# Kernel tuning notes

Measured on AMD Instinct MI355X. Metric: run time of the kernel, lower is better.

The kernel has to match this reference:

```python
import jax, jax.numpy as jnp
import numpy as np

N = 100000   # nodes
E = 1600000  # edges
G = 64       # graphs in batch
C = 8        # num_classes
H = 128      # hidden dim


def _lin(k, out_f, in_f):
    return jax.random.normal(k, (out_f, in_f), jnp.float32) * (1.0 / np.sqrt(in_f))


def setup_inputs() -> dict:
    key = jax.random.key(0)
    ks = jax.random.split(key, 16)
    x = jax.random.normal(ks[0], (N, 5), jnp.float32)
    edge_index = jax.random.randint(ks[1], (2, E), 0, N)
    batch = jnp.sort(jax.random.randint(ks[2], (N,), 0, G))
    exinfo = jax.random.normal(ks[3], (G, 10), jnp.float32)
    return {
        "x": x, "edge_index": edge_index, "batch": batch, "exinfo": exinfo,
        # GraphConv1: 3 -> 128 (PyG GraphConv: lin_root(x) + lin_rel(scatter_add(x_j)))
        "Wroot1": _lin(ks[4], H, 3), "Wrel1": _lin(ks[5], H, 3), "brel1": jnp.zeros((H,), jnp.float32),
        # GraphConv2: 128 -> 128
        "Wroot2": _lin(ks[6], H, H), "Wrel2": _lin(ks[7], H, H), "brel2": jnp.zeros((H,), jnp.float32),
        # MLP head
        "W1": _lin(ks[8], 64, 2 * H + 10), "b1": jnp.zeros((64,), jnp.float32),
        "W2": _lin(ks[9], 32, 64), "b2": jnp.zeros((32,), jnp.float32),
        "W3": _lin(ks[10], C, 32), "b3": jnp.zeros((C,), jnp.float32),
    }


def _graph_conv(x, src, dst, Wroot, Wrel, brel):
    # PyG GraphConv (aggr='add'): out_i = Wrel @ sum_{j->i} x_j + brel + Wroot @ x_i
    agg = jax.ops.segment_sum(x[src], dst, num_segments=x.shape[0])  # [N, F]
    return agg @ Wrel.T + brel + x @ Wroot.T


def reference(x, edge_index, batch, exinfo,
              Wroot1, Wrel1, brel1, Wroot2, Wrel2, brel2,
              W1, b1, W2, b2, W3, b3):
    xs = x[:, 2:5]                              # data.x[:, 2:5]
    src, dst = edge_index[0], edge_index[1]
    x1 = jax.nn.relu(_graph_conv(xs, src, dst, Wroot1, Wrel1, brel1))   # [N, 128]
    x2 = jax.nn.relu(_graph_conv(x1, src, dst, Wroot2, Wrel2, brel2))   # [N, 128]
    h = jnp.concatenate([x1, x2], axis=-1)      # [N, 256]
    g = jax.ops.segment_max(h, batch, num_segments=G)  # global max pool [G, 256]
    g = jnp.concatenate([g, exinfo], axis=-1)   # [G, 266]
    g = jax.nn.relu(g @ W1.T + b1)
    g = jax.nn.relu(g @ W2.T + b2)
    return jax.nn.log_softmax(g @ W3.T + b3, axis=-1)
```

## Files before the change

### kernel.cpp

```cpp
#include <hip/hip_runtime.h>

#define N_NODES 100000
#define N_EDGES 1600000
#define NG 64
#define NC 8
#define HD 128

#define BUCKET_SHIFT 8
#define NB ((N_NODES + 255) >> 8)
#define NCHUNK 256
#define EPC (N_EDGES / NCHUNK)

typedef __attribute__((ext_vector_type(8))) __bf16 bf16x8;
typedef __attribute__((ext_vector_type(4))) float f32x4;
typedef __attribute__((ext_vector_type(2))) float f32x2;


__global__ void bin_hist_k(const int* __restrict__ dst, int* __restrict__ hist) {
  __shared__ int lh[NB];
  int c = blockIdx.x, t = threadIdx.x;
  for (int b = t; b < NB; b += 256) lh[b] = 0;
  __syncthreads();
  int e0 = c * EPC;
  for (int i = t; i < EPC; i += 256) atomicAdd(&lh[dst[e0 + i] >> BUCKET_SHIFT], 1);
  __syncthreads();
  for (int b = t; b < NB; b += 256) hist[c * NB + b] = lh[b];
}

__launch_bounds__(512)
__global__ void base_k(const int* __restrict__ hist, int* __restrict__ bucket_base,
                       int* __restrict__ row_ptr) {
  __shared__ int tot[512];
  int t = threadIdx.x;
  int s = 0;
  if (t < NB)
    for (int c = 0; c < NCHUNK; c++) s += hist[c * NB + t];
  tot[t] = s;
  __syncthreads();
  for (int off = 1; off < 512; off <<= 1) {
    int v = (t >= off) ? tot[t - off] : 0;
    __syncthreads();
    tot[t] += v;
    __syncthreads();
  }
  if (t < NB) bucket_base[t] = tot[t] - s;
  if (t == 0) { bucket_base[NB] = N_EDGES; row_ptr[N_NODES] = N_EDGES; }
}

__global__ void chunk_scan_k(int* __restrict__ hist, const int* __restrict__ bucket_base) {
  int b = blockIdx.x, lane = threadIdx.x;
  int carry = bucket_base[b];
#pragma unroll
  for (int it = 0; it < NCHUNK / 64; it++) {
    int c = it * 64 + lane;
    int v = hist[c * NB + b];
    int s = v;
#pragma unroll
    for (int off = 1; off < 64; off <<= 1) {
      int u = __shfl_up(s, off);
      if (lane >= off) s += u;
    }
    hist[c * NB + b] = carry + s - v;
    carry += __shfl(s, 63);
  }
}

__global__ void scatter_k(const int* __restrict__ src, const int* __restrict__ dst,
                          const int* __restrict__ hist, unsigned int* __restrict__ pairs) {
  __shared__ int loff[NB];
  int c = blockIdx.x, t = threadIdx.x;
  for (int b = t; b < NB; b += 256) loff[b] = hist[c * NB + b];
  __syncthreads();
  int e0 = c * EPC;
  for (int i = t; i < EPC; i += 256) {
    int d = dst[e0 + i], s = src[e0 + i];
    int pos = atomicAdd(&loff[d >> BUCKET_SHIFT], 1);
    pairs[pos] = ((unsigned int)s << 8) | (unsigned int)(d & 255);
  }
}

__global__ void bucket_csr_k(const unsigned int* __restrict__ pairs,
                             const int* __restrict__ bucket_base,
                             int* __restrict__ row_ptr, int* __restrict__ csr) {
  __shared__ int cnt[256];
  __shared__ int start[256];
  __shared__ int wsum[4];
  int b = blockIdx.x, t = threadIdx.x, lane = t & 63, wid = t >> 6;
  int nb0 = b << BUCKET_SHIFT;
  int beg = bucket_base[b], end = bucket_base[b + 1];
  cnt[t] = 0;
  __syncthreads();
  for (int i = beg + t; i < end; i += 256) atomicAdd(&cnt[pairs[i] & 255u], 1);
  __syncthreads();
  int v = cnt[t];
  int s = v;
#pragma unroll
  for (int off = 1; off < 64; off <<= 1) {
    int u = __shfl_up(s, off);
    if (lane >= off) s += u;
  }
  if (lane == 63) wsum[wid] = s;
  __syncthreads();
  if (t == 0) {
    int a = 0;
    for (int j = 0; j < 4; j++) { int x = wsum[j]; wsum[j] = a; a += x; }
  }
  __syncthreads();
  int excl = wsum[wid] + s - v;
  start[t] = excl;
  if (nb0 + t < N_NODES) row_ptr[nb0 + t] = beg + excl;
  cnt[t] = 0;
  __syncthreads();
  for (int i = beg + t; i < end; i += 256) {
    unsigned int p = pairs[i];
    int li = p & 255u;
    int pos = beg + start[li] + atomicAdd(&cnt[li], 1);
    csr[pos] = (int)(p >> 8);
  }
}


__global__ void pack_xs_k(const float* __restrict__ x, float4* __restrict__ xs4) {
  int i = blockIdx.x * 256 + threadIdx.x;
  if (i < N_NODES) {
    const float* xp = x + (size_t)i * 5;
    xs4[i] = make_float4(xp[2], xp[3], xp[4], 0.f);
  }
}


__global__ void conv1_k(const float4* __restrict__ xs4, const int* __restrict__ row_ptr,
                        const int* __restrict__ csr, const float* __restrict__ Wroot1,
                        const float* __restrict__ Wrel1, const float* __restrict__ brel1,
                        __bf16* __restrict__ xcat) {
  int node = blockIdx.x * 4 + (threadIdx.x >> 6);
  if (node >= N_NODES) return;
  int lane = threadIdx.x & 63;
  int beg = row_ptr[node], end = row_ptr[node + 1];
  float a0 = 0.f, a1 = 0.f, a2 = 0.f;
  for (int e = beg + lane; e < end; e += 64) {
    float4 v = xs4[csr[e]];
    a0 += v.x; a1 += v.y; a2 += v.z;
  }
#pragma unroll
  for (int m = 1; m < 64; m <<= 1) {
    a0 += __shfl_xor(a0, m);
    a1 += __shfl_xor(a1, m);
    a2 += __shfl_xor(a2, m);
  }
  float4 rv = xs4[node];
  __bf16* orow = xcat + (size_t)node * 256 + 128;
#pragma unroll
  for (int hh = 0; hh < 2; hh++) {
    int h = lane + hh * 64;
    float v = brel1[h]
            + a0 * Wrel1[h * 3 + 0] + a1 * Wrel1[h * 3 + 1] + a2 * Wrel1[h * 3 + 2]
            + rv.x * Wroot1[h * 3 + 0] + rv.y * Wroot1[h * 3 + 1] + rv.z * Wroot1[h * 3 + 2];
    orow[h] = (__bf16)fmaxf(v, 0.f);
  }
}


#define LDROW(s) (*((const uint4*)(xcat + (size_t)(s) * 256 + 128) + f))
#define ACC8(u) \
  acc2[0] += (f32x2){__uint_as_float((u).x << 16), __uint_as_float((u).x & 0xffff0000u)}; \
  acc2[1] += (f32x2){__uint_as_float((u).y << 16), __uint_as_float((u).y & 0xffff0000u)}; \
  acc2[2] += (f32x2){__uint_as_float((u).z << 16), __uint_as_float((u).z & 0xffff0000u)}; \
  acc2[3] += (f32x2){__uint_as_float((u).w << 16), __uint_as_float((u).w & 0xffff0000u)};

__global__ void agg2_k(const int* __restrict__ row_ptr, const int* __restrict__ csr,
                       __bf16* xcat) {
  int node = blockIdx.x * 4 + (threadIdx.x >> 6);
  if (node >= N_NODES) return;
  int lane = threadIdx.x & 63;
  int g = lane >> 4, f = lane & 15;
  int beg = row_ptr[node], end = row_ptr[node + 1];
  int deg = end - beg;
  int idx = (lane < deg) ? csr[beg + lane] : 0;
  f32x2 acc2[4];
#pragma unroll
  for (int k = 0; k < 4; k++) acc2[k] = (f32x2){0.f, 0.f};
  int dmain = deg < 64 ? deg : 64;
  int j = 0;
  for (; j + 16 <= dmain; j += 16) {
    int s0 = __shfl(idx, j + g);
    int s1 = __shfl(idx, j + 4 + g);
    int s2 = __shfl(idx, j + 8 + g);
    int s3 = __shfl(idx, j + 12 + g);
    uint4 u0 = LDROW(s0);
    uint4 u1 = LDROW(s1);
    uint4 u2 = LDROW(s2);
    uint4 u3 = LDROW(s3);
    ACC8(u0) ACC8(u1) ACC8(u2) ACC8(u3)
  }
  if (j + 8 <= dmain) {
    int s0 = __shfl(idx, j + g);
    int s1 = __shfl(idx, j + 4 + g);
    uint4 u0 = LDROW(s0);
    uint4 u1 = LDROW(s1);
    ACC8(u0) ACC8(u1)
    j += 8;
  }
  if (j + 4 <= dmain) {
    int s0 = __shfl(idx, j + g);
    uint4 u0 = LDROW(s0);
    ACC8(u0)
    j += 4;
  }
  {
    int rem = dmain - j;
    int s0 = __shfl(idx, j + (g < rem ? g : 0));
    if (g < rem) {
      uint4 u0 = LDROW(s0);
      ACC8(u0)
    }
  }
  for (int e = beg + 64; e < end; e += 4) {
    int m = end - e;
    int s0 = csr[e + (g < m ? g : 0)];
    if (g < m) {
      uint4 u0 = LDROW(s0);
      ACC8(u0)
    }
  }
#pragma unroll
  for (int k = 0; k < 4; k++) {
    acc2[k].x += __shfl_xor(acc2[k].x, 16);
    acc2[k].y += __shfl_xor(acc2[k].y, 16);
    acc2[k].x += __shfl_xor(acc2[k].x, 32);
    acc2[k].y += __shfl_xor(acc2[k].y, 32);
  }
  if (g == 0) {
    uint4 o;
    o.x = (__float_as_uint((float)(__bf16)acc2[0].x) >> 16) | (__float_as_uint((float)(__bf16)acc2[0].y) & 0xffff0000u);
    o.y = (__float_as_uint((float)(__bf16)acc2[1].x) >> 16) | (__float_as_uint((float)(__bf16)acc2[1].y) & 0xffff0000u);
    o.z = (__float_as_uint((float)(__bf16)acc2[2].x) >> 16) | (__float_as_uint((float)(__bf16)acc2[2].y) & 0xffff0000u);
    o.w = (__float_as_uint((float)(__bf16)acc2[3].x) >> 16) | (__float_as_uint((float)(__bf16)acc2[3].y) & 0xffff0000u);
    *((uint4*)(xcat + (size_t)node * 256) + f) = o;
  }
}


__global__ void build_wc_k(const float* __restrict__ Wrel2, const float* __restrict__ Wroot2,
                           __bf16* __restrict__ Wc) {
  int i = blockIdx.x * 256 + threadIdx.x;
  int h = i >> 8, k = i & 255;
  float v = (k < 128) ? Wrel2[h * 128 + k] : Wroot2[h * 128 + (k - 128)];
  Wc[i] = (__bf16)v;
}


__launch_bounds__(512, 4)
__global__ void gemm2_k(const __bf16* __restrict__ xcat, const __bf16* __restrict__ Wc,
                        const float* __restrict__ brel2, const int* __restrict__ batch,
                        unsigned int* __restrict__ gout) {
  __shared__ char Blds[128 * 256 * 2];
  int t = threadIdx.x;
  for (int i = t; i < 4096; i += 512) {
    uint4 v = ((const uint4*)Wc)[i];
    int byte = i * 16;
    int sw = byte ^ (((byte >> 9) & 7) << 4);
    *(uint4*)(Blds + sw) = v;
  }
  __syncthreads();
  int wid = t >> 6, lane = t & 63;
  int nb = (blockIdx.x * 8 + wid) * 32;
  if (nb >= N_NODES) return;
  int r = lane & 15, ko = lane >> 4;
  const __bf16* arow0 = xcat + (size_t)(nb + r) * 256 + ko * 8;
  const __bf16* arow1 = arow0 + 16 * 256;
  f32x4 acc0[8], acc1[8];
#pragma unroll
  for (int i = 0; i < 8; i++) {
    acc0[i] = (f32x4){0.f, 0.f, 0.f, 0.f};
    acc1[i] = (f32x4){0.f, 0.f, 0.f, 0.f};
  }
#pragma unroll
  for (int kb = 0; kb < 256; kb += 32) {
    bf16x8 a0 = *(const bf16x8*)(arow0 + kb);
    bf16x8 a1 = *(const bf16x8*)(arow1 + kb);
#pragma unroll
    for (int ht = 0; ht < 8; ht++) {
      int h = ht * 16 + r;
      int byte = h * 512 + ko * 16 + kb * 2;
      bf16x8 b = *(const bf16x8*)(Blds + (byte ^ ((r & 7) << 4)));
      acc0[ht] = __builtin_amdgcn_mfma_f32_16x16x32_bf16(a0, b, acc0[ht], 0, 0, 0);
      acc1[ht] = __builtin_amdgcn_mfma_f32_16x16x32_bf16(a1, b, acc1[ht], 0, 0, 0);
    }
  }
  int gfirst = batch[nb], glast = batch[nb + 31];
  if (gfirst == glast) {
    unsigned int* gp = gout + gfirst * 256 + 128;
#pragma unroll
    for (int ht = 0; ht < 8; ht++) {
      float bias = brel2[ht * 16 + r];
      float m = 0.f;
#pragma unroll
      for (int rr = 0; rr < 4; rr++) {
        m = fmaxf(m, acc0[ht][rr] + bias);
        m = fmaxf(m, acc1[ht][rr] + bias);
      }
      m = fmaxf(m, __shfl_xor(m, 16));
      m = fmaxf(m, __shfl_xor(m, 32));
      if (ko == 0) atomicMax(&gp[ht * 16 + r], __float_as_uint(m));
    }
  } else {
    int g0[4], g1[4];
#pragma unroll
    for (int rr = 0; rr < 4; rr++) {
      g0[rr] = batch[nb + ko * 4 + rr];
      g1[rr] = batch[nb + 16 + ko * 4 + rr];
    }
#pragma unroll
    for (int ht = 0; ht < 8; ht++) {
      int h = ht * 16 + r;
      float bias = brel2[h];
#pragma unroll
      for (int rr = 0; rr < 4; rr++) {
        atomicMax(&gout[g0[rr] * 256 + 128 + h],
                  __float_as_uint(fmaxf(acc0[ht][rr] + bias, 0.f)));
        atomicMax(&gout[g1[rr] * 256 + 128 + h],
                  __float_as_uint(fmaxf(acc1[ht][rr] + bias, 0.f)));
      }
    }
  }
}


__global__ void segmax1_k(const __bf16* __restrict__ xcat, const int* __restrict__ batch,
                          unsigned int* __restrict__ g) {
  int t = threadIdx.x;
  int f = t & 63;
  int s = t >> 6;
  int n0 = blockIdx.x * 256;
  float m0 = 0.f, m1 = 0.f;
  int cur = -1;
  int n1 = n0 + 256 < N_NODES ? n0 + 256 : N_NODES;
  for (int n = n0 + s; n < n1; n += 4) {
    int b = batch[n];
    if (b != cur) {
      if (cur >= 0) {
        atomicMax(&g[cur * 256 + 2 * f], __float_as_uint(m0));
        atomicMax(&g[cur * 256 + 2 * f + 1], __float_as_uint(m1));
      }
      cur = b; m0 = 0.f; m1 = 0.f;
    }
    unsigned int u = ((const unsigned int*)(xcat + (size_t)n * 256 + 128))[f];
    m0 = fmaxf(m0, __uint_as_float(u << 16));
    m1 = fmaxf(m1, __uint_as_float(u & 0xffff0000u));
  }
  if (cur >= 0) {
    atomicMax(&g[cur * 256 + 2 * f], __float_as_uint(m0));
    atomicMax(&g[cur * 256 + 2 * f + 1], __float_as_uint(m1));
  }
}


__global__ void head1_k(const float* __restrict__ g, const float* __restrict__ exinfo,
                        const float* __restrict__ W1, const float* __restrict__ b1,
                        float* __restrict__ g1) {
  int gg = blockIdx.x;
  int t = threadIdx.x;
  int c = t >> 2, q = t & 3;
  const float* w = W1 + c * 266;
  const float* gr = g + gg * 256;
  float s = 0.f;
  for (int k = q * 64; k < q * 64 + 64; k++) s += gr[k] * w[k];
  if (q == 0) {
    const float* er = exinfo + gg * 10;
    for (int k = 0; k < 10; k++) s += er[k] * w[256 + k];
    s += b1[c];
  }
  s += __shfl_xor(s, 1);
  s += __shfl_xor(s, 2);
  if (q == 0) g1[gg * 64 + c] = fmaxf(s, 0.f);
}

__global__ void head2_k(const float* __restrict__ g1, const float* __restrict__ W2,
                        const float* __restrict__ b2, const float* __restrict__ W3,
                        const float* __restrict__ b3, float* __restrict__ out) {
  __shared__ float s1[64 * 64];
  __shared__ float s2[64 * 32];
  int t = threadIdx.x;
  for (int i = t; i < 4096; i += 256) s1[i] = g1[i];
  __syncthreads();
  for (int o = t; o < 2048; o += 256) {
    int r = o >> 5, c = o & 31;
    float s = b2[c];
    for (int k = 0; k < 64; k++) s += s1[r * 64 + k] * W2[c * 64 + k];
    s2[r * 32 + c] = fmaxf(s, 0.f);
  }
  __syncthreads();
  if (t < 64) {
    float lg[8];
#pragma unroll
    for (int c = 0; c < 8; c++) {
      float s = b3[c];
      for (int k = 0; k < 32; k++) s += s2[t * 32 + k] * W3[c * 32 + k];
      lg[c] = s;
    }
    float mx = lg[0];
#pragma unroll
    for (int c = 1; c < 8; c++) mx = fmaxf(mx, lg[c]);
    float se = 0.f;
#pragma unroll
    for (int c = 0; c < 8; c++) se += expf(lg[c] - mx);
    float lse = mx + logf(se);
#pragma unroll
    for (int c = 0; c < 8; c++) out[t * 8 + c] = lg[c] - lse;
  }
}


extern "C" void kernel_launch(void* const* d_in, const int* in_sizes, int n_in,
                              void* d_out, int out_size, void* d_ws, size_t ws_size,
                              hipStream_t stream) {
  const float* x      = (const float*)d_in[0];
  const int*   edge   = (const int*)d_in[1];
  const int*   batch  = (const int*)d_in[2];
  const float* exinfo = (const float*)d_in[3];
  const float* Wroot1 = (const float*)d_in[4];
  const float* Wrel1  = (const float*)d_in[5];
  const float* brel1  = (const float*)d_in[6];
  const float* Wroot2 = (const float*)d_in[7];
  const float* Wrel2  = (const float*)d_in[8];
  const float* brel2  = (const float*)d_in[9];
  const float* W1     = (const float*)d_in[10];
  const float* b1     = (const float*)d_in[11];
  const float* W2     = (const float*)d_in[12];
  const float* b2     = (const float*)d_in[13];
  const float* W3     = (const float*)d_in[14];
  const float* b3     = (const float*)d_in[15];
  const int* src = edge;
  const int* dst = edge + N_EDGES;

  char* p = (char*)d_ws;
  auto alloc = [&](size_t bytes) {
    char* q = p;
    p += (bytes + 511) & ~(size_t)511;
    return (void*)q;
  };
  __bf16*       Wc          = (__bf16*)alloc(128 * 256 * 2);
  unsigned int* g           = (unsigned int*)alloc(64 * 256 * 4);
  float*        g1          = (float*)alloc(64 * 64 * 4);
  float4*       xs4         = (float4*)alloc((size_t)N_NODES * 16);
  int*          hist        = (int*)alloc((size_t)NCHUNK * NB * 4);
  int*          bucket_base = (int*)alloc((size_t)(NB + 1) * 4);
  int*          row_ptr     = (int*)alloc((size_t)(N_NODES + 1) * 4);
  int*          csr         = (int*)alloc((size_t)N_EDGES * 4);
  __bf16*       xcat        = (__bf16*)alloc((size_t)N_NODES * 256 * 2);
  unsigned int* pairs       = (unsigned int*)alloc((size_t)N_EDGES * 4);

  hipMemsetAsync(g, 0, 64 * 256 * 4, stream);
  build_wc_k<<<128, 256, 0, stream>>>(Wrel2, Wroot2, Wc);
  pack_xs_k<<<NB, 256, 0, stream>>>(x, xs4);
  bin_hist_k<<<NCHUNK, 256, 0, stream>>>(dst, hist);
  base_k<<<1, 512, 0, stream>>>(hist, bucket_base, row_ptr);
  chunk_scan_k<<<NB, 64, 0, stream>>>(hist, bucket_base);
  scatter_k<<<NCHUNK, 256, 0, stream>>>(src, dst, hist, pairs);
  bucket_csr_k<<<NB, 256, 0, stream>>>(pairs, bucket_base, row_ptr, csr);
  conv1_k<<<25000, 256, 0, stream>>>(xs4, row_ptr, csr, Wroot1, Wrel1, brel1, xcat);
  agg2_k<<<25000, 256, 0, stream>>>(row_ptr, csr, xcat);
  gemm2_k<<<391, 512, 0, stream>>>(xcat, Wc, brel2, batch, g);
  segmax1_k<<<NB, 256, 0, stream>>>(xcat, batch, g);
  head1_k<<<64, 256, 0, stream>>>((const float*)g, exinfo, W1, b1, g1);
  head2_k<<<1, 256, 0, stream>>>(g1, W2, b2, W3, b3, (float*)d_out);
}
```

Baseline: 215.4 us.

## Gather layer-1 features in FP8 for aggregation, fuse init kernels, parallelize bucket sum

conv1 now also writes an FP8 (e4m3) copy of x1, and the second-layer neighbour aggregation gathers these 128-byte rows instead of 256-byte bf16 rows. This halves the bytes moved by the random gather, but adds quantisation error to the aggregated features. The memset, weight packing and xs packing are merged into one init kernel. The serial per-bucket histogram sum in the single-block scan is replaced by a parallel reduction kernel feeding a smaller scan.

```diff
diff --git a/kernel.cpp b/kernel.cpp
--- a/kernel.cpp
+++ b/kernel.cpp
@@ -15,6 +15,44 @@
 typedef __attribute__((ext_vector_type(4))) float f32x4;
 typedef __attribute__((ext_vector_type(2))) float f32x2;
 
+#if defined(__has_builtin)
+#if __has_builtin(__builtin_amdgcn_cvt_pk_f32_fp8)
+#define HAVE_FP8_CVT 1
+#endif
+#endif
+
+__device__ inline unsigned int f32_to_e4m3(float v) {
+  unsigned int b = __float_as_uint(v);
+  b += 0x00080000u;
+  unsigned int e = b >> 23;
+  if (e < 121) return 0u;
+  unsigned int q = (e > 135) ? 0x7Eu : (((e - 120) << 3) | ((b >> 20) & 7u));
+  return q > 0x7Eu ? 0x7Eu : q;
+}
+
+__device__ inline float e4m3f(unsigned int t) {
+  unsigned int e = (t >> 3) & 0xFu;
+  unsigned int r = ((t & 0x80u) << 24) | ((e + 120u) << 23) | ((t & 7u) << 20);
+  return e ? __uint_as_float(r) : 0.f;
+}
+
+
+__global__ void init_k(const float* __restrict__ x, const float* __restrict__ Wrel2,
+                       const float* __restrict__ Wroot2, float4* __restrict__ xs4,
+                       __bf16* __restrict__ Wc, unsigned int* __restrict__ g) {
+  int i = blockIdx.x * 256 + threadIdx.x;
+  if (i < 64 * 256) g[i] = 0u;
+  if (i < 32768) {
+    int h = i >> 8, k = i & 255;
+    float v = (k < 128) ? Wrel2[h * 128 + k] : Wroot2[h * 128 + (k - 128)];
+    Wc[i] = (__bf16)v;
+  }
+  if (i < N_NODES) {
+    const float* xp = x + (size_t)i * 5;
+    xs4[i] = make_float4(xp[2], xp[3], xp[4], 0.f);
+  }
+}
+
 
 __global__ void bin_hist_k(const int* __restrict__ dst, int* __restrict__ hist) {
   __shared__ int lh[NB];
@@ -27,23 +65,33 @@
   for (int b = t; b < NB; b += 256) hist[c * NB + b] = lh[b];
 }
 
+
+__global__ void bucket_sum_k(const int* __restrict__ hist, int* __restrict__ tot) {
+  __shared__ int ws[4];
+  int b = blockIdx.x, t = threadIdx.x, lane = t & 63, wid = t >> 6;
+  int v = hist[t * NB + b];
+#pragma unroll
+  for (int off = 1; off < 64; off <<= 1) v += __shfl_xor(v, off);
+  if (lane == 0) ws[wid] = v;
+  __syncthreads();
+  if (t == 0) tot[b] = ws[0] + ws[1] + ws[2] + ws[3];
+}
+
 __launch_bounds__(512)
-__global__ void base_k(const int* __restrict__ hist, int* __restrict__ bucket_base,
-                       int* __restrict__ row_ptr) {
-  __shared__ int tot[512];
+__global__ void scan391_k(const int* __restrict__ tot, int* __restrict__ bucket_base,
+                          int* __restrict__ row_ptr) {
+  __shared__ int sm[512];
   int t = threadIdx.x;
-  int s = 0;
-  if (t < NB)
-    for (int c = 0; c < NCHUNK; c++) s += hist[c * NB + t];
-  tot[t] = s;
+  int s = (t < NB) ? tot[t] : 0;
+  sm[t] = s;
   __syncthreads();
   for (int off = 1; off < 512; off <<= 1) {
-    int v = (t >= off) ? tot[t - off] : 0;
+    int v = (t >= off) ? sm[t - off] : 0;
     __syncthreads();
-    tot[t] += v;
+    sm[t] += v;
     __syncthreads();
   }
-  if (t < NB) bucket_base[t] = tot[t] - s;
+  if (t < NB) bucket_base[t] = sm[t] - s;
   if (t == 0) { bucket_base[NB] = N_EDGES; row_ptr[N_NODES] = N_EDGES; }
 }
 
@@ -120,19 +168,10 @@
 }
 
 
-__global__ void pack_xs_k(const float* __restrict__ x, float4* __restrict__ xs4) {
-  int i = blockIdx.x * 256 + threadIdx.x;
-  if (i < N_NODES) {
-    const float* xp = x + (size_t)i * 5;
-    xs4[i] = make_float4(xp[2], xp[3], xp[4], 0.f);
-  }
-}
-
-
 __global__ void conv1_k(const float4* __restrict__ xs4, const int* __restrict__ row_ptr,
                         const int* __restrict__ csr, const float* __restrict__ Wroot1,
                         const float* __restrict__ Wrel1, const float* __restrict__ brel1,
-                        __bf16* __restrict__ xcat) {
+                        __bf16* __restrict__ xcat, unsigned char* __restrict__ x1q) {
   int node = blockIdx.x * 4 + (threadIdx.x >> 6);
   if (node >= N_NODES) return;
   int lane = threadIdx.x & 63;
@@ -150,103 +189,99 @@
   }
   float4 rv = xs4[node];
   __bf16* orow = xcat + (size_t)node * 256 + 128;
+  unsigned char* qrow = x1q + (size_t)node * 128;
 #pragma unroll
   for (int hh = 0; hh < 2; hh++) {
     int h = lane + hh * 64;
     float v = brel1[h]
             + a0 * Wrel1[h * 3 + 0] + a1 * Wrel1[h * 3 + 1] + a2 * Wrel1[h * 3 + 2]
             + rv.x * Wroot1[h * 3 + 0] + rv.y * Wroot1[h * 3 + 1] + rv.z * Wroot1[h * 3 + 2];
-    orow[h] = (__bf16)fmaxf(v, 0.f);
-  }
-}
-
-
-#define LDROW(s) (*((const uint4*)(xcat + (size_t)(s) * 256 + 128) + f))
-#define ACC8(u) \
-  acc2[0] += (f32x2){__uint_as_float((u).x << 16), __uint_as_float((u).x & 0xffff0000u)}; \
-  acc2[1] += (f32x2){__uint_as_float((u).y << 16), __uint_as_float((u).y & 0xffff0000u)}; \
-  acc2[2] += (f32x2){__uint_as_float((u).z << 16), __uint_as_float((u).z & 0xffff0000u)}; \
-  acc2[3] += (f32x2){__uint_as_float((u).w << 16), __uint_as_float((u).w & 0xffff0000u)};
+    v = fmaxf(v, 0.f);
+    orow[h] = (__bf16)v;
+    qrow[h] = (unsigned char)f32_to_e4m3(v);
+  }
+}
+
+
+#ifdef HAVE_FP8_CVT
+#define ACCD(dw, base) { f32x2 lo_ = __builtin_amdgcn_cvt_pk_f32_fp8((dw), 0); \
+                         f32x2 hi_ = __builtin_amdgcn_cvt_pk_f32_fp8((dw), 1); \
+                         acc[(base)+0] += lo_[0]; acc[(base)+1] += lo_[1];     \
+                         acc[(base)+2] += hi_[0]; acc[(base)+3] += hi_[1]; }
+#else
+#define ACCD(dw, base) { acc[(base)+0] += e4m3f((dw) & 0xFFu);        \
+                         acc[(base)+1] += e4m3f(((dw) >> 8) & 0xFFu); \
+                         acc[(base)+2] += e4m3f(((dw) >> 16) & 0xFFu);\
+                         acc[(base)+3] += e4m3f((dw) >> 24); }
+#endif
+#define ACCQ(u) { ACCD((u).x, 0) ACCD((u).y, 4) ACCD((u).z, 8) ACCD((u).w, 12) }
+#define LDQ(s) (*((const uint4*)(x1q + (size_t)(s) * 128) + f))
 
 __global__ void agg2_k(const int* __restrict__ row_ptr, const int* __restrict__ csr,
-                       __bf16* xcat) {
+                       const unsigned char* __restrict__ x1q, __bf16* xcat) {
   int node = blockIdx.x * 4 + (threadIdx.x >> 6);
   if (node >= N_NODES) return;
   int lane = threadIdx.x & 63;
-  int g = lane >> 4, f = lane & 15;
+  int g = lane >> 3, f = lane & 7;
   int beg = row_ptr[node], end = row_ptr[node + 1];
   int deg = end - beg;
   int idx = (lane < deg) ? csr[beg + lane] : 0;
-  f32x2 acc2[4];
-#pragma unroll
-  for (int k = 0; k < 4; k++) acc2[k] = (f32x2){0.f, 0.f};
+  float acc[16];
+#pragma unroll
+  for (int k = 0; k < 16; k++) acc[k] = 0.f;
   int dmain = deg < 64 ? deg : 64;
   int j = 0;
   for (; j + 16 <= dmain; j += 16) {
     int s0 = __shfl(idx, j + g);
-    int s1 = __shfl(idx, j + 4 + g);
-    int s2 = __shfl(idx, j + 8 + g);
-    int s3 = __shfl(idx, j + 12 + g);
-    uint4 u0 = LDROW(s0);
-    uint4 u1 = LDROW(s1);
-    uint4 u2 = LDROW(s2);
-    uint4 u3 = LDROW(s3);
-    ACC8(u0) ACC8(u1) ACC8(u2) ACC8(u3)
+    int s1 = __shfl(idx, j + 8 + g);
+    uint4 u0 = LDQ(s0);
+    uint4 u1 = LDQ(s1);
+    ACCQ(u0) ACCQ(u1)
   }
   if (j + 8 <= dmain) {
     int s0 = __shfl(idx, j + g);
-    int s1 = __shfl(idx, j + 4 + g);
-    uint4 u0 = LDROW(s0);
-    uint4 u1 = LDROW(s1);
-    ACC8(u0) ACC8(u1)
+    uint4 u0 = LDQ(s0);
+    ACCQ(u0)
     j += 8;
-  }
-  if (j + 4 <= dmain) {
-    int s0 = __shfl(idx, j + g);
-    uint4 u0 = LDROW(s0);
-    ACC8(u0)
-    j += 4;
   }
   {
     int rem = dmain - j;
     int s0 = __shfl(idx, j + (g < rem ? g : 0));
     if (g < rem) {
-      uint4 u0 = LDROW(s0);
-      ACC8(u0)
-    }
-  }
-  for (int e = beg + 64; e < end; e += 4) {
+      uint4 u0 = LDQ(s0);
+      ACCQ(u0)
+    }
+  }
+  for (int e = beg + 64; e < end; e += 8) {
     int m = end - e;
     int s0 = csr[e + (g < m ? g : 0)];
     if (g < m) {
-      uint4 u0 = LDROW(s0);
-      ACC8(u0)
-    }
-  }
-#pragma unroll
-  for (int k = 0; k < 4; k++) {
-    acc2[k].x += __shfl_xor(acc2[k].x, 16);
-    acc2[k].y += __shfl_xor(acc2[k].y, 16);
-    acc2[k].x += __shfl_xor(acc2[k].x, 32);
-    acc2[k].y += __shfl_xor(acc2[k].y, 32);
-  }
-  if (g == 0) {
+      uint4 u0 = LDQ(s0);
+      ACCQ(u0)
+    }
+  }
+#pragma unroll
+  for (int k = 0; k < 16; k++) {
+    acc[k] += __shfl_xor(acc[k], 8);
+    acc[k] += __shfl_xor(acc[k], 16);
+    acc[k] += __shfl_xor(acc[k], 32);
+  }
+  int L = lane, fsel = L >> 1, half = L & 1;
+  float vals[8];
+#pragma unroll
+  for (int jj = 0; jj < 8; jj++) {
+    float va = __shfl(acc[jj], fsel);
+    float vb = __shfl(acc[8 + jj], fsel);
+    vals[jj] = half ? vb : va;
+  }
+  if (L < 16) {
     uint4 o;
-    o.x = (__float_as_uint((float)(__bf16)acc2[0].x) >> 16) | (__float_as_uint((float)(__bf16)acc2[0].y) & 0xffff0000u);
-    o.y = (__float_as_uint((float)(__bf16)acc2[1].x) >> 16) | (__float_as_uint((float)(__bf16)acc2[1].y) & 0xffff0000u);
-    o.z = (__float_as_uint((float)(__bf16)acc2[2].x) >> 16) | (__float_as_uint((float)(__bf16)acc2[2].y) & 0xffff0000u);
-    o.w = (__float_as_uint((float)(__bf16)acc2[3].x) >> 16) | (__float_as_uint((float)(__bf16)acc2[3].y) & 0xffff0000u);
-    *((uint4*)(xcat + (size_t)node * 256) + f) = o;
-  }
-}
-
-
-__global__ void build_wc_k(const float* __restrict__ Wrel2, const float* __restrict__ Wroot2,
-                           __bf16* __restrict__ Wc) {
-  int i = blockIdx.x * 256 + threadIdx.x;
-  int h = i >> 8, k = i & 255;
-  float v = (k < 128) ? Wrel2[h * 128 + k] : Wroot2[h * 128 + (k - 128)];
-  Wc[i] = (__bf16)v;
+    o.x = (__float_as_uint((float)(__bf16)vals[0]) >> 16) | (__float_as_uint((float)(__bf16)vals[1]) & 0xffff0000u);
+    o.y = (__float_as_uint((float)(__bf16)vals[2]) >> 16) | (__float_as_uint((float)(__bf16)vals[3]) & 0xffff0000u);
+    o.z = (__float_as_uint((float)(__bf16)vals[4]) >> 16) | (__float_as_uint((float)(__bf16)vals[5]) & 0xffff0000u);
+    o.w = (__float_as_uint((float)(__bf16)vals[6]) >> 16) | (__float_as_uint((float)(__bf16)vals[7]) & 0xffff0000u);
+    *((uint4*)(xcat + (size_t)node * 256) + L) = o;
+  }
 }
 
 
@@ -440,27 +475,28 @@
     p += (bytes + 511) & ~(size_t)511;
     return (void*)q;
   };
-  __bf16*       Wc          = (__bf16*)alloc(128 * 256 * 2);
-  unsigned int* g           = (unsigned int*)alloc(64 * 256 * 4);
-  float*        g1          = (float*)alloc(64 * 64 * 4);
-  float4*       xs4         = (float4*)alloc((size_t)N_NODES * 16);
-  int*          hist        = (int*)alloc((size_t)NCHUNK * NB * 4);
-  int*          bucket_base = (int*)alloc((size_t)(NB + 1) * 4);
-  int*          row_ptr     = (int*)alloc((size_t)(N_NODES + 1) * 4);
-  int*          csr         = (int*)alloc((size_t)N_EDGES * 4);
-  __bf16*       xcat        = (__bf16*)alloc((size_t)N_NODES * 256 * 2);
-  unsigned int* pairs       = (unsigned int*)alloc((size_t)N_EDGES * 4);
-
-  hipMemsetAsync(g, 0, 64 * 256 * 4, stream);
-  build_wc_k<<<128, 256, 0, stream>>>(Wrel2, Wroot2, Wc);
-  pack_xs_k<<<NB, 256, 0, stream>>>(x, xs4);
+  __bf16*        Wc          = (__bf16*)alloc(128 * 256 * 2);
+  unsigned int*  g           = (unsigned int*)alloc(64 * 256 * 4);
+  float*         g1          = (float*)alloc(64 * 64 * 4);
+  float4*        xs4         = (float4*)alloc((size_t)N_NODES * 16);
+  int*           hist        = (int*)alloc((size_t)NCHUNK * NB * 4);
+  int*           btot        = (int*)alloc((size_t)NB * 4);
+  int*           bucket_base = (int*)alloc((size_t)(NB + 1) * 4);
+  int*           row_ptr     = (int*)alloc((size_t)(N_NODES + 1) * 4);
+  int*           csr         = (int*)alloc((size_t)N_EDGES * 4);
+  __bf16*        xcat        = (__bf16*)alloc((size_t)N_NODES * 256 * 2);
+  unsigned char* x1q         = (unsigned char*)alloc((size_t)N_NODES * 128);
+  unsigned int*  pairs       = (unsigned int*)alloc((size_t)N_EDGES * 4);
+
+  init_k<<<NB, 256, 0, stream>>>(x, Wrel2, Wroot2, xs4, Wc, g);
   bin_hist_k<<<NCHUNK, 256, 0, stream>>>(dst, hist);
-  base_k<<<1, 512, 0, stream>>>(hist, bucket_base, row_ptr);
+  bucket_sum_k<<<NB, 256, 0, stream>>>(hist, btot);
+  scan391_k<<<1, 512, 0, stream>>>(btot, bucket_base, row_ptr);
   chunk_scan_k<<<NB, 64, 0, stream>>>(hist, bucket_base);
   scatter_k<<<NCHUNK, 256, 0, stream>>>(src, dst, hist, pairs);
   bucket_csr_k<<<NB, 256, 0, stream>>>(pairs, bucket_base, row_ptr, csr);
-  conv1_k<<<25000, 256, 0, stream>>>(xs4, row_ptr, csr, Wroot1, Wrel1, brel1, xcat);
-  agg2_k<<<25000, 256, 0, stream>>>(row_ptr, csr, xcat);
+  conv1_k<<<25000, 256, 0, stream>>>(xs4, row_ptr, csr, Wroot1, Wrel1, brel1, xcat, x1q);
+  agg2_k<<<25000, 256, 0, stream>>>(row_ptr, csr, x1q, xcat);
   gemm2_k<<<391, 512, 0, stream>>>(xcat, Wc, brel2, batch, g);
   segmax1_k<<<NB, 256, 0, stream>>>(xcat, batch, g);
   head1_k<<<64, 256, 0, stream>>>((const float*)g, exinfo, W1, b1, g1);
```

Measured after the change: 226.2 us. 1.05x slower.
